# Kernel optimization log

Measured on AMD Instinct MI355X. Metric: run time of the kernel, lower is better.

## Reference

```python
import jax, jax.numpy as jnp
import numpy as np

N_ANCHORS = 4_000_000
N_VALID = 2_000_000
EPS = 1e-10


def setup_inputs() -> dict:
    key = jax.random.key(0)
    k1, k2, k3, k4, k5, k6 = jax.random.split(key, 6)
    bbox_pred = jax.random.normal(k1, (1, N_ANCHORS, 4), dtype=jnp.float32)
    class_logits = jax.random.normal(k2, (1, N_ANCHORS, 2), dtype=jnp.float32)
    sigma_pred = jax.random.uniform(k3, (1, N_ANCHORS, 4), dtype=jnp.float32)  # positive variance head
    gt_bbox = jax.random.normal(k4, (1, N_ANCHORS, 4), dtype=jnp.float32)
    gt_anchor_label = jax.random.randint(k5, (1, N_ANCHORS), 0, 2, dtype=jnp.int64)
    valid_idx = jnp.sort(jax.random.randint(k6, (N_VALID,), 0, N_ANCHORS, dtype=jnp.int64))
    return {
        "bbox_pred": bbox_pred,
        "class_logits": class_logits,
        "sigma_pred": sigma_pred,
        "gt_bbox": gt_bbox,
        "gt_anchor_label": gt_anchor_label,
        "valid_idx": valid_idx,
    }


def reference(bbox_pred, class_logits, sigma_pred, gt_bbox, gt_anchor_label, valid_idx):
    # Gather valid anchors (batch index 0, as in original code)
    lbl_v = gt_anchor_label[0][valid_idx]            # [V]
    logits_v = class_logits[0][valid_idx]            # [V, 2]
    p = bbox_pred[0][valid_idx]                      # [V, 4]
    t = gt_bbox[0][valid_idx]                        # [V, 4]
    s = sigma_pred[0][valid_idx]                     # [V, 4]

    # Classification loss: mean cross-entropy over valid anchors
    logp = jax.nn.log_softmax(logits_v, axis=-1)     # [V, 2]
    class_loss = -jnp.take_along_axis(logp, lbl_v[:, None], axis=1).mean()

    pos = (lbl_v == 1)                               # [V] bool
    sq = 0.5 * (p - t) ** 2                          # [V, 4]
    per_bbox = (sq / (EPS + s)).sum(axis=-1)         # [V]
    per_sigma = (0.5 * jnp.log(EPS + s)).sum(axis=-1)  # [V]
    per_neg = (1.0 / (EPS + s)).sum(axis=-1)         # [V]

    n_pos = pos.sum().astype(jnp.float32)
    n_neg = (~pos).sum().astype(jnp.float32)

    reg_loss_bbox = jnp.where(pos, per_bbox, 0.0).sum() / n_pos
    reg_loss_sigma = jnp.where(pos, per_sigma, 0.0).sum() / n_pos
    reg_loss_neg = jnp.where(pos, 0.0, per_neg).sum() / n_neg

    # Faithful to original bug: loss_bbox_only is '=' (not '+='), so it keeps
    # only the LAST positive anchor's squared-error sum, divided by n_pos.
    last_pos = jnp.max(jnp.where(pos, jnp.arange(pos.shape[0]), -1))
    reg_loss_bbox_only = sq.sum(axis=-1)[last_pos] / n_pos

    return (class_loss, reg_loss_bbox, reg_loss_sigma, reg_loss_neg, reg_loss_bbox_only)
```

## Files before the change

### kernel.cpp

```cpp
#include <hip/hip_runtime.h>
#include <math.h>

#define EPS 1e-10f
#define MAIN_BLOCK 256
#define MAX_BLOCKS 2048


__global__ __launch_bounds__(MAIN_BLOCK) void rpn_loss_main(
    const float4* __restrict__ bbox,
    const float2* __restrict__ logits,
    const float4* __restrict__ sigma,
    const float4* __restrict__ gt,
    const int*    __restrict__ labels,
    const int*    __restrict__ vidx,
    int V,
    double* __restrict__ partials,
    int* __restrict__ pnpos,
    int* __restrict__ plastpos)
{
    double cls_s = 0.0, bbox_s = 0.0, sig_s = 0.0, neg_s = 0.0;
    int npos = 0;
    int lastpos = -1;

    int tid    = blockIdx.x * blockDim.x + threadIdx.x;
    int stride = gridDim.x * blockDim.x;

    for (int i = tid; i < V; i += stride) {
        int idx = vidx[i];
        int lbl = labels[idx];

        float2 lg  = logits[idx];
        float l_p  = lbl ? lg.y : lg.x;
        float l_o  = lbl ? lg.x : lg.y;
        float d    = l_o - l_p;
        float closs = (d > 0.0f) ? (d + log1pf(expf(-d))) : log1pf(expf(d));
        cls_s += (double)closs;

        float4 p = bbox[idx];
        float4 t = gt[idx];
        float4 s = sigma[idx];

        float dx = p.x - t.x, dy = p.y - t.y, dz = p.z - t.z, dw = p.w - t.w;
        float i0 = 1.0f / (EPS + s.x);
        float i1 = 1.0f / (EPS + s.y);
        float i2 = 1.0f / (EPS + s.z);
        float i3 = 1.0f / (EPS + s.w);

        if (lbl == 1) {
            float per_bbox = 0.5f * dx * dx * i0 + 0.5f * dy * dy * i1
                           + 0.5f * dz * dz * i2 + 0.5f * dw * dw * i3;
            float per_sigma = 0.5f * (logf(EPS + s.x) + logf(EPS + s.y)
                                    + logf(EPS + s.z) + logf(EPS + s.w));
            bbox_s += (double)per_bbox;
            sig_s  += (double)per_sigma;
            npos   += 1;
            lastpos = i;
        } else {
            neg_s += (double)(i0 + i1 + i2 + i3);
        }
    }

    for (int off = 32; off > 0; off >>= 1) {
        cls_s  += __shfl_down(cls_s,  off);
        bbox_s += __shfl_down(bbox_s, off);
        sig_s  += __shfl_down(sig_s,  off);
        neg_s  += __shfl_down(neg_s,  off);
        npos   += __shfl_down(npos,   off);
        int lp  = __shfl_down(lastpos, off);
        lastpos = lp > lastpos ? lp : lastpos;
    }

    __shared__ double s_acc[4][4];
    __shared__ int    s_np[4];
    __shared__ int    s_lp[4];
    int wave = threadIdx.x >> 6;
    if ((threadIdx.x & 63) == 0) {
        s_acc[wave][0] = cls_s;
        s_acc[wave][1] = bbox_s;
        s_acc[wave][2] = sig_s;
        s_acc[wave][3] = neg_s;
        s_np[wave] = npos;
        s_lp[wave] = lastpos;
    }
    __syncthreads();
    if (threadIdx.x == 0) {
        double c = 0, b = 0, sg = 0, ng = 0;
        int np = 0, lp = -1;
        for (int w = 0; w < 4; ++w) {
            c  += s_acc[w][0];
            b  += s_acc[w][1];
            sg += s_acc[w][2];
            ng += s_acc[w][3];
            np += s_np[w];
            lp  = s_lp[w] > lp ? s_lp[w] : lp;
        }
        partials[blockIdx.x * 4 + 0] = c;
        partials[blockIdx.x * 4 + 1] = b;
        partials[blockIdx.x * 4 + 2] = sg;
        partials[blockIdx.x * 4 + 3] = ng;
        pnpos[blockIdx.x]    = np;
        plastpos[blockIdx.x] = lp;
    }
}

__global__ __launch_bounds__(256) void finalize_kernel(
    const double* __restrict__ partials,
    const int* __restrict__ pnpos,
    const int* __restrict__ plastpos,
    int nb,
    const int* __restrict__ vidx,
    const float4* __restrict__ bbox,
    const float4* __restrict__ gt,
    int V,
    float* __restrict__ out)
{
    double cls_s = 0.0, bbox_s = 0.0, sig_s = 0.0, neg_s = 0.0;
    int npos = 0, lastpos = -1;

    for (int i = threadIdx.x; i < nb; i += 256) {
        cls_s  += partials[i * 4 + 0];
        bbox_s += partials[i * 4 + 1];
        sig_s  += partials[i * 4 + 2];
        neg_s  += partials[i * 4 + 3];
        npos   += pnpos[i];
        int lp  = plastpos[i];
        lastpos = lp > lastpos ? lp : lastpos;
    }

    for (int off = 32; off > 0; off >>= 1) {
        cls_s  += __shfl_down(cls_s,  off);
        bbox_s += __shfl_down(bbox_s, off);
        sig_s  += __shfl_down(sig_s,  off);
        neg_s  += __shfl_down(neg_s,  off);
        npos   += __shfl_down(npos,   off);
        int lp  = __shfl_down(lastpos, off);
        lastpos = lp > lastpos ? lp : lastpos;
    }

    __shared__ double s_acc[4][4];
    __shared__ int    s_np[4];
    __shared__ int    s_lp[4];
    int wave = threadIdx.x >> 6;
    if ((threadIdx.x & 63) == 0) {
        s_acc[wave][0] = cls_s;
        s_acc[wave][1] = bbox_s;
        s_acc[wave][2] = sig_s;
        s_acc[wave][3] = neg_s;
        s_np[wave] = npos;
        s_lp[wave] = lastpos;
    }
    __syncthreads();

    if (threadIdx.x == 0) {
        double c = 0, b = 0, sg = 0, ng = 0;
        int np = 0, lp = -1;
        for (int w = 0; w < 4; ++w) {
            c  += s_acc[w][0];
            b  += s_acc[w][1];
            sg += s_acc[w][2];
            ng += s_acc[w][3];
            np += s_np[w];
            lp  = s_lp[w] > lp ? s_lp[w] : lp;
        }
        float n_pos = (float)np;

        out[0] = (float)(c / (double)V);
        out[1] = (float)(b / (double)np);
        out[2] = (float)(sg / (double)np);
        out[3] = (float)(ng / (double)(V - np));

        float v4 = 0.0f;
        if (lp >= 0) {
            int idx = vidx[lp];
            float4 pp = bbox[idx];
            float4 tt = gt[idx];
            float ddx = pp.x - tt.x, ddy = pp.y - tt.y;
            float ddz = pp.z - tt.z, ddw = pp.w - tt.w;
            v4 = 0.5f * (ddx * ddx + ddy * ddy + ddz * ddz + ddw * ddw) / n_pos;
        }
        out[4] = v4;
    }
}

extern "C" void kernel_launch(void* const* d_in, const int* in_sizes, int n_in,
                              void* d_out, int out_size, void* d_ws, size_t ws_size,
                              hipStream_t stream) {
    const float* bbox_pred    = (const float*)d_in[0];
    const float* class_logits = (const float*)d_in[1];
    const float* sigma_pred   = (const float*)d_in[2];
    const float* gt_bbox      = (const float*)d_in[3];
    const int*   gt_label     = (const int*)d_in[4];
    const int*   valid_idx    = (const int*)d_in[5];

    int V = in_sizes[5];

    double* partials = (double*)d_ws;
    int*    pnpos    = (int*)((char*)d_ws + MAX_BLOCKS * 4 * sizeof(double));
    int*    plastpos = pnpos + MAX_BLOCKS;

    int blocks = (V + MAIN_BLOCK - 1) / MAIN_BLOCK;
    if (blocks > MAX_BLOCKS) blocks = MAX_BLOCKS;

    rpn_loss_main<<<blocks, MAIN_BLOCK, 0, stream>>>(
        (const float4*)bbox_pred,
        (const float2*)class_logits,
        (const float4*)sigma_pred,
        (const float4*)gt_bbox,
        gt_label, valid_idx, V, partials, pnpos, plastpos);

    finalize_kernel<<<1, 256, 0, stream>>>(
        partials, pnpos, plastpos, blocks,
        valid_idx,
        (const float4*)bbox_pred,
        (const float4*)gt_bbox,
        V, (float*)d_out);
}
```

Baseline: 234.1 us.

## Replace indexed gather with histogram count plus dense streaming pass over anchors

Adds a first pass that histograms valid indices into a per-anchor count array with atomics and finds the last positive index. A second pass streams all anchor arrays contiguously and weights each anchor's loss terms by its count, replacing random gathers with coalesced reads. If the workspace is too small, a fallback kernel instead batches four gathered elements per thread to raise memory-level parallelism. The count path reads every anchor, including unused ones, and adds a 16MB memset and atomic traffic.

```diff
diff --git a/kernel.cpp b/kernel.cpp
--- a/kernel.cpp
+++ b/kernel.cpp
@@ -2,43 +2,69 @@
 #include <math.h>
 
 #define EPS 1e-10f
+#define P1_BLOCKS 2048
+#define P2_BLOCKS 2048
 #define MAIN_BLOCK 256
-#define MAX_BLOCKS 2048
-
-
-__global__ __launch_bounds__(MAIN_BLOCK) void rpn_loss_main(
+
+
+__global__ __launch_bounds__(MAIN_BLOCK) void pass1_count(
+    const int* __restrict__ vidx,
+    const int* __restrict__ labels,
+    int V,
+    int* __restrict__ count,
+    int* __restrict__ g_lastpos)
+{
+    int tid    = blockIdx.x * blockDim.x + threadIdx.x;
+    int stride = gridDim.x * blockDim.x;
+    int lastpos = -1;
+
+    for (int i = tid; i < V; i += stride) {
+        int idx = vidx[i];
+        atomicAdd(&count[idx], 1);
+        if (labels[idx] == 1) lastpos = i;
+    }
+
+    for (int off = 32; off > 0; off >>= 1) {
+        int lp = __shfl_down(lastpos, off);
+        lastpos = lp > lastpos ? lp : lastpos;
+    }
+    if ((threadIdx.x & 63) == 0 && lastpos >= 0)
+        atomicMax(g_lastpos, lastpos);
+}
+
+__global__ __launch_bounds__(MAIN_BLOCK) void pass2_stream(
     const float4* __restrict__ bbox,
     const float2* __restrict__ logits,
     const float4* __restrict__ sigma,
     const float4* __restrict__ gt,
     const int*    __restrict__ labels,
-    const int*    __restrict__ vidx,
-    int V,
+    const int*    __restrict__ count,
+    int N,
     double* __restrict__ partials,
-    int* __restrict__ pnpos,
-    int* __restrict__ plastpos)
+    int* __restrict__ pnpos)
 {
     double cls_s = 0.0, bbox_s = 0.0, sig_s = 0.0, neg_s = 0.0;
     int npos = 0;
-    int lastpos = -1;
 
     int tid    = blockIdx.x * blockDim.x + threadIdx.x;
     int stride = gridDim.x * blockDim.x;
 
-    for (int i = tid; i < V; i += stride) {
-        int idx = vidx[i];
-        int lbl = labels[idx];
-
-        float2 lg  = logits[idx];
-        float l_p  = lbl ? lg.y : lg.x;
-        float l_o  = lbl ? lg.x : lg.y;
-        float d    = l_o - l_p;
+    for (int a = tid; a < N; a += stride) {
+        int    c  = count[a];
+        int    l  = labels[a];
+        float2 lg = logits[a];
+        float4 p  = bbox[a];
+        float4 t  = gt[a];
+        float4 s  = sigma[a];
+
+        if (c == 0) continue;
+        double dc = (double)c;
+
+        float l_p = l ? lg.y : lg.x;
+        float l_o = l ? lg.x : lg.y;
+        float d   = l_o - l_p;
         float closs = (d > 0.0f) ? (d + log1pf(expf(-d))) : log1pf(expf(d));
-        cls_s += (double)closs;
-
-        float4 p = bbox[idx];
-        float4 t = gt[idx];
-        float4 s = sigma[idx];
+        cls_s += dc * (double)closs;
 
         float dx = p.x - t.x, dy = p.y - t.y, dz = p.z - t.z, dw = p.w - t.w;
         float i0 = 1.0f / (EPS + s.x);
@@ -46,17 +72,16 @@
         float i2 = 1.0f / (EPS + s.z);
         float i3 = 1.0f / (EPS + s.w);
 
-        if (lbl == 1) {
+        if (l == 1) {
             float per_bbox = 0.5f * dx * dx * i0 + 0.5f * dy * dy * i1
                            + 0.5f * dz * dz * i2 + 0.5f * dw * dw * i3;
             float per_sigma = 0.5f * (logf(EPS + s.x) + logf(EPS + s.y)
                                     + logf(EPS + s.z) + logf(EPS + s.w));
-            bbox_s += (double)per_bbox;
-            sig_s  += (double)per_sigma;
-            npos   += 1;
-            lastpos = i;
+            bbox_s += dc * (double)per_bbox;
+            sig_s  += dc * (double)per_sigma;
+            npos   += c;
         } else {
-            neg_s += (double)(i0 + i1 + i2 + i3);
+            neg_s += dc * (double)(i0 + i1 + i2 + i3);
         }
     }
 
@@ -66,13 +91,10 @@
         sig_s  += __shfl_down(sig_s,  off);
         neg_s  += __shfl_down(neg_s,  off);
         npos   += __shfl_down(npos,   off);
-        int lp  = __shfl_down(lastpos, off);
-        lastpos = lp > lastpos ? lp : lastpos;
     }
 
     __shared__ double s_acc[4][4];
     __shared__ int    s_np[4];
-    __shared__ int    s_lp[4];
     int wave = threadIdx.x >> 6;
     if ((threadIdx.x & 63) == 0) {
         s_acc[wave][0] = cls_s;
@@ -80,34 +102,31 @@
         s_acc[wave][2] = sig_s;
         s_acc[wave][3] = neg_s;
         s_np[wave] = npos;
-        s_lp[wave] = lastpos;
     }
     __syncthreads();
     if (threadIdx.x == 0) {
         double c = 0, b = 0, sg = 0, ng = 0;
-        int np = 0, lp = -1;
+        int np = 0;
         for (int w = 0; w < 4; ++w) {
             c  += s_acc[w][0];
             b  += s_acc[w][1];
             sg += s_acc[w][2];
             ng += s_acc[w][3];
             np += s_np[w];
-            lp  = s_lp[w] > lp ? s_lp[w] : lp;
         }
         partials[blockIdx.x * 4 + 0] = c;
         partials[blockIdx.x * 4 + 1] = b;
         partials[blockIdx.x * 4 + 2] = sg;
         partials[blockIdx.x * 4 + 3] = ng;
-        pnpos[blockIdx.x]    = np;
-        plastpos[blockIdx.x] = lp;
-    }
-}
-
-__global__ __launch_bounds__(256) void finalize_kernel(
+        pnpos[blockIdx.x] = np;
+    }
+}
+
+__global__ __launch_bounds__(256) void finalize2_kernel(
     const double* __restrict__ partials,
     const int* __restrict__ pnpos,
-    const int* __restrict__ plastpos,
     int nb,
+    const int* __restrict__ g_lastpos,
     const int* __restrict__ vidx,
     const float4* __restrict__ bbox,
     const float4* __restrict__ gt,
@@ -115,7 +134,7 @@
     float* __restrict__ out)
 {
     double cls_s = 0.0, bbox_s = 0.0, sig_s = 0.0, neg_s = 0.0;
-    int npos = 0, lastpos = -1;
+    int npos = 0;
 
     for (int i = threadIdx.x; i < nb; i += 256) {
         cls_s  += partials[i * 4 + 0];
@@ -123,8 +142,6 @@
         sig_s  += partials[i * 4 + 2];
         neg_s  += partials[i * 4 + 3];
         npos   += pnpos[i];
-        int lp  = plastpos[i];
-        lastpos = lp > lastpos ? lp : lastpos;
     }
 
     for (int off = 32; off > 0; off >>= 1) {
@@ -133,13 +150,10 @@
         sig_s  += __shfl_down(sig_s,  off);
         neg_s  += __shfl_down(neg_s,  off);
         npos   += __shfl_down(npos,   off);
-        int lp  = __shfl_down(lastpos, off);
-        lastpos = lp > lastpos ? lp : lastpos;
     }
 
     __shared__ double s_acc[4][4];
     __shared__ int    s_np[4];
-    __shared__ int    s_lp[4];
     int wave = threadIdx.x >> 6;
     if ((threadIdx.x & 63) == 0) {
         s_acc[wave][0] = cls_s;
@@ -147,22 +161,20 @@
         s_acc[wave][2] = sig_s;
         s_acc[wave][3] = neg_s;
         s_np[wave] = npos;
-        s_lp[wave] = lastpos;
     }
     __syncthreads();
 
     if (threadIdx.x == 0) {
         double c = 0, b = 0, sg = 0, ng = 0;
-        int np = 0, lp = -1;
+        int np = 0;
         for (int w = 0; w < 4; ++w) {
             c  += s_acc[w][0];
             b  += s_acc[w][1];
             sg += s_acc[w][2];
             ng += s_acc[w][3];
             np += s_np[w];
-            lp  = s_lp[w] > lp ? s_lp[w] : lp;
-        }
-        float n_pos = (float)np;
+        }
+        int lp = *g_lastpos;
 
         out[0] = (float)(c / (double)V);
         out[1] = (float)(b / (double)np);
@@ -176,7 +188,141 @@
             float4 tt = gt[idx];
             float ddx = pp.x - tt.x, ddy = pp.y - tt.y;
             float ddz = pp.z - tt.z, ddw = pp.w - tt.w;
-            v4 = 0.5f * (ddx * ddx + ddy * ddy + ddz * ddz + ddw * ddw) / n_pos;
+            v4 = 0.5f * (ddx * ddx + ddy * ddy + ddz * ddz + ddw * ddw) / (float)np;
+        }
+        out[4] = v4;
+    }
+}
+
+#define FB_BATCH 4
+#define FB_MAX_BLOCKS 4096
+
+__global__ __launch_bounds__(MAIN_BLOCK) void rpn_loss_main_fb(
+    const float4* __restrict__ bbox, const float2* __restrict__ logits,
+    const float4* __restrict__ sigma, const float4* __restrict__ gt,
+    const int* __restrict__ labels, const int* __restrict__ vidx, int V,
+    double* __restrict__ partials, int* __restrict__ pnpos, int* __restrict__ plastpos)
+{
+    double cls_s = 0.0, bbox_s = 0.0, sig_s = 0.0, neg_s = 0.0;
+    int npos = 0, lastpos = -1;
+    int base = blockIdx.x * (MAIN_BLOCK * FB_BATCH) + threadIdx.x;
+
+    int idxs[FB_BATCH]; bool vld[FB_BATCH];
+#pragma unroll
+    for (int k = 0; k < FB_BATCH; ++k) {
+        int i = base + k * MAIN_BLOCK;
+        vld[k] = (i < V);
+        idxs[k] = vld[k] ? vidx[i] : 0;
+    }
+    int lbl[FB_BATCH]; float2 lg[FB_BATCH]; float4 p[FB_BATCH], t[FB_BATCH], s[FB_BATCH];
+#pragma unroll
+    for (int k = 0; k < FB_BATCH; ++k) lbl[k] = labels[idxs[k]];
+#pragma unroll
+    for (int k = 0; k < FB_BATCH; ++k) lg[k] = logits[idxs[k]];
+#pragma unroll
+    for (int k = 0; k < FB_BATCH; ++k) p[k] = bbox[idxs[k]];
+#pragma unroll
+    for (int k = 0; k < FB_BATCH; ++k) t[k] = gt[idxs[k]];
+#pragma unroll
+    for (int k = 0; k < FB_BATCH; ++k) s[k] = sigma[idxs[k]];
+
+#pragma unroll
+    for (int k = 0; k < FB_BATCH; ++k) {
+        if (!vld[k]) continue;
+        float l_p = lbl[k] ? lg[k].y : lg[k].x;
+        float l_o = lbl[k] ? lg[k].x : lg[k].y;
+        float d = l_o - l_p;
+        float closs = (d > 0.0f) ? (d + log1pf(expf(-d))) : log1pf(expf(d));
+        cls_s += (double)closs;
+        float dx = p[k].x - t[k].x, dy = p[k].y - t[k].y;
+        float dz = p[k].z - t[k].z, dw = p[k].w - t[k].w;
+        float i0 = 1.0f / (EPS + s[k].x), i1 = 1.0f / (EPS + s[k].y);
+        float i2 = 1.0f / (EPS + s[k].z), i3 = 1.0f / (EPS + s[k].w);
+        if (lbl[k] == 1) {
+            bbox_s += (double)(0.5f * dx * dx * i0 + 0.5f * dy * dy * i1
+                             + 0.5f * dz * dz * i2 + 0.5f * dw * dw * i3);
+            sig_s += (double)(0.5f * (logf(EPS + s[k].x) + logf(EPS + s[k].y)
+                                    + logf(EPS + s[k].z) + logf(EPS + s[k].w)));
+            npos += 1;
+            lastpos = base + k * MAIN_BLOCK;
+        } else {
+            neg_s += (double)(i0 + i1 + i2 + i3);
+        }
+    }
+
+    for (int off = 32; off > 0; off >>= 1) {
+        cls_s += __shfl_down(cls_s, off); bbox_s += __shfl_down(bbox_s, off);
+        sig_s += __shfl_down(sig_s, off); neg_s += __shfl_down(neg_s, off);
+        npos += __shfl_down(npos, off);
+        int lp = __shfl_down(lastpos, off);
+        lastpos = lp > lastpos ? lp : lastpos;
+    }
+    __shared__ double s_acc[4][4]; __shared__ int s_np[4]; __shared__ int s_lp[4];
+    int wave = threadIdx.x >> 6;
+    if ((threadIdx.x & 63) == 0) {
+        s_acc[wave][0] = cls_s; s_acc[wave][1] = bbox_s;
+        s_acc[wave][2] = sig_s; s_acc[wave][3] = neg_s;
+        s_np[wave] = npos; s_lp[wave] = lastpos;
+    }
+    __syncthreads();
+    if (threadIdx.x == 0) {
+        double c = 0, b = 0, sg = 0, ng = 0; int np = 0, lp = -1;
+        for (int w = 0; w < 4; ++w) {
+            c += s_acc[w][0]; b += s_acc[w][1]; sg += s_acc[w][2]; ng += s_acc[w][3];
+            np += s_np[w]; lp = s_lp[w] > lp ? s_lp[w] : lp;
+        }
+        partials[blockIdx.x * 4 + 0] = c; partials[blockIdx.x * 4 + 1] = b;
+        partials[blockIdx.x * 4 + 2] = sg; partials[blockIdx.x * 4 + 3] = ng;
+        pnpos[blockIdx.x] = np; plastpos[blockIdx.x] = lp;
+    }
+}
+
+__global__ __launch_bounds__(256) void finalize_fb(
+    const double* __restrict__ partials, const int* __restrict__ pnpos,
+    const int* __restrict__ plastpos, int nb, const int* __restrict__ vidx,
+    const float4* __restrict__ bbox, const float4* __restrict__ gt,
+    int V, float* __restrict__ out)
+{
+    double cls_s = 0.0, bbox_s = 0.0, sig_s = 0.0, neg_s = 0.0;
+    int npos = 0, lastpos = -1;
+    for (int i = threadIdx.x; i < nb; i += 256) {
+        cls_s += partials[i * 4 + 0]; bbox_s += partials[i * 4 + 1];
+        sig_s += partials[i * 4 + 2]; neg_s += partials[i * 4 + 3];
+        npos += pnpos[i];
+        int lp = plastpos[i]; lastpos = lp > lastpos ? lp : lastpos;
+    }
+    for (int off = 32; off > 0; off >>= 1) {
+        cls_s += __shfl_down(cls_s, off); bbox_s += __shfl_down(bbox_s, off);
+        sig_s += __shfl_down(sig_s, off); neg_s += __shfl_down(neg_s, off);
+        npos += __shfl_down(npos, off);
+        int lp = __shfl_down(lastpos, off);
+        lastpos = lp > lastpos ? lp : lastpos;
+    }
+    __shared__ double s_acc[4][4]; __shared__ int s_np[4]; __shared__ int s_lp[4];
+    int wave = threadIdx.x >> 6;
+    if ((threadIdx.x & 63) == 0) {
+        s_acc[wave][0] = cls_s; s_acc[wave][1] = bbox_s;
+        s_acc[wave][2] = sig_s; s_acc[wave][3] = neg_s;
+        s_np[wave] = npos; s_lp[wave] = lastpos;
+    }
+    __syncthreads();
+    if (threadIdx.x == 0) {
+        double c = 0, b = 0, sg = 0, ng = 0; int np = 0, lp = -1;
+        for (int w = 0; w < 4; ++w) {
+            c += s_acc[w][0]; b += s_acc[w][1]; sg += s_acc[w][2]; ng += s_acc[w][3];
+            np += s_np[w]; lp = s_lp[w] > lp ? s_lp[w] : lp;
+        }
+        out[0] = (float)(c / (double)V);
+        out[1] = (float)(b / (double)np);
+        out[2] = (float)(sg / (double)np);
+        out[3] = (float)(ng / (double)(V - np));
+        float v4 = 0.0f;
+        if (lp >= 0) {
+            int idx = vidx[lp];
+            float4 pp = bbox[idx]; float4 tt = gt[idx];
+            float ddx = pp.x - tt.x, ddy = pp.y - tt.y;
+            float ddz = pp.z - tt.z, ddw = pp.w - tt.w;
+            v4 = 0.5f * (ddx * ddx + ddy * ddy + ddz * ddz + ddw * ddw) / (float)np;
         }
         out[4] = v4;
     }
@@ -192,26 +338,50 @@
     const int*   gt_label     = (const int*)d_in[4];
     const int*   valid_idx    = (const int*)d_in[5];
 
+    int N = in_sizes[4];
     int V = in_sizes[5];
 
-    double* partials = (double*)d_ws;
-    int*    pnpos    = (int*)((char*)d_ws + MAX_BLOCKS * 4 * sizeof(double));
-    int*    plastpos = pnpos + MAX_BLOCKS;
-
-    int blocks = (V + MAIN_BLOCK - 1) / MAIN_BLOCK;
-    if (blocks > MAX_BLOCKS) blocks = MAX_BLOCKS;
-
-    rpn_loss_main<<<blocks, MAIN_BLOCK, 0, stream>>>(
-        (const float4*)bbox_pred,
-        (const float2*)class_logits,
-        (const float4*)sigma_pred,
-        (const float4*)gt_bbox,
-        gt_label, valid_idx, V, partials, pnpos, plastpos);
-
-    finalize_kernel<<<1, 256, 0, stream>>>(
-        partials, pnpos, plastpos, blocks,
-        valid_idx,
-        (const float4*)bbox_pred,
-        (const float4*)gt_bbox,
-        V, (float*)d_out);
-}
+    size_t count_bytes = (size_t)N * sizeof(int);
+    size_t need = count_bytes + 64
+                + (size_t)P2_BLOCKS * 4 * sizeof(double)
+                + (size_t)P2_BLOCKS * sizeof(int);
+
+    if (ws_size >= need) {
+        int*    count     = (int*)d_ws;
+        char*   base      = (char*)d_ws + count_bytes;
+        int*    g_lastpos = (int*)base;
+        double* partials  = (double*)(base + 64);
+        int*    pnpos     = (int*)(base + 64 + P2_BLOCKS * 4 * sizeof(double));
+
+        hipMemsetAsync(count, 0, count_bytes, stream);
+        hipMemsetAsync(g_lastpos, 0xFF, sizeof(int), stream);
+
+        pass1_count<<<P1_BLOCKS, MAIN_BLOCK, 0, stream>>>(
+            valid_idx, gt_label, V, count, g_lastpos);
+
+        pass2_stream<<<P2_BLOCKS, MAIN_BLOCK, 0, stream>>>(
+            (const float4*)bbox_pred, (const float2*)class_logits,
+            (const float4*)sigma_pred, (const float4*)gt_bbox,
+            gt_label, count, N, partials, pnpos);
+
+        finalize2_kernel<<<1, 256, 0, stream>>>(
+            partials, pnpos, P2_BLOCKS, g_lastpos, valid_idx,
+            (const float4*)bbox_pred, (const float4*)gt_bbox, V, (float*)d_out);
+    } else {
+        double* partials = (double*)d_ws;
+        int*    pnpos    = (int*)((char*)d_ws + FB_MAX_BLOCKS * 4 * sizeof(double));
+        int*    plastpos = pnpos + FB_MAX_BLOCKS;
+
+        int blocks = (V + MAIN_BLOCK * FB_BATCH - 1) / (MAIN_BLOCK * FB_BATCH);
+        if (blocks > FB_MAX_BLOCKS) blocks = FB_MAX_BLOCKS;
+
+        rpn_loss_main_fb<<<blocks, MAIN_BLOCK, 0, stream>>>(
+            (const float4*)bbox_pred, (const float2*)class_logits,
+            (const float4*)sigma_pred, (const float4*)gt_bbox,
+            gt_label, valid_idx, V, partials, pnpos, plastpos);
+
+        finalize_fb<<<1, 256, 0, stream>>>(
+            partials, pnpos, plastpos, blocks, valid_idx,
+            (const float4*)bbox_pred, (const float4*)gt_bbox, V, (float*)d_out);
+    }
+}
```

New measurement: 355.9 us. +52.0%, slower.
